# Optimization experiments

Hardware: AMD Instinct MI355X
Metric: run time of the kernel (lower is better)

## Reference

```python
import jax, jax.numpy as jnp
import numpy as np

N_HEADS = 16
NEG_INF = -1e9


def setup_inputs() -> dict:
    key = jax.random.key(0)
    k1, k2 = jax.random.split(key)
    B, T, C = 2, 2048, 1024
    x = jax.random.normal(k1, (B, T, C), dtype=jnp.float32)
    mask = jnp.ones((B, T, T), dtype=bool)  # padding mask, broadcastable to (B,T,T)
    W_qkv = jax.random.normal(k2, (3 * C, C), dtype=jnp.float32) * (C ** -0.5)
    b_qkv = jnp.zeros((3 * C,), dtype=jnp.float32)
    return {"x": x, "mask": mask, "W_qkv": W_qkv, "b_qkv": b_qkv}


def reference(x, mask, W_qkv, b_qkv):
    B, T, C = x.shape
    H = N_HEADS
    hd = C // H
    scale = jnp.asarray(C, jnp.float32) ** -0.5  # registered buffer 'scale'

    qkv = x @ W_qkv.T + b_qkv  # (B,T,3C)
    q, k, v = jnp.split(qkv, 3, axis=2)
    q = q.reshape(B, T, H, hd).transpose(0, 2, 1, 3)  # (B,H,T,hd)
    k = k.reshape(B, T, H, hd).transpose(0, 2, 1, 3)
    v = v.reshape(B, T, H, hd).transpose(0, 2, 1, 3)

    # NOTE: original code divides by scale = C**-0.5, i.e. multiplies by sqrt(C).
    att = jnp.einsum("bhqd,bhkd->bhqk", q, k) / scale  # (B,H,T,T)

    causal = jnp.tril(jnp.ones((T, T), dtype=bool))  # causal_mask buffer
    m = mask[:, None, :, :] & causal  # (B,1,T,T) & (T,T) -> (B,1,T,T)
    att = jnp.where(m, att, NEG_INF)
    att = jax.nn.softmax(att, axis=-1)

    y = jnp.einsum("bhqk,bhkd->bhqd", att, v)  # (B,H,T,hd)
    return y.transpose(0, 2, 1, 3).reshape(B, T, C)
```

## Files before the change

### kernel.cpp

```cpp
#include <hip/hip_runtime.h>


#define T_SEQ 2048
#define CDIM  1024
#define NH    16
#define HD    64

typedef short bf16x8 __attribute__((ext_vector_type(8)));
typedef float f32x4  __attribute__((ext_vector_type(4)));

#if defined(__has_builtin) && __has_builtin(__builtin_amdgcn_exp2f)
#define EXP2F __builtin_amdgcn_exp2f
#else
#define EXP2F exp2f
#endif

#define QSCALE 46.16624130844683f

__device__ __forceinline__ ushort f2bf(float x) {
    uint32_t u = __float_as_uint(x);
    return (ushort)((u + 0x7FFFu + ((u >> 16) & 1u)) >> 16);
}
__device__ __forceinline__ float bf2f(ushort h) {
    return __uint_as_float(((uint32_t)h) << 16);
}
__device__ __forceinline__ uint2 pack4(ushort a, ushort b, ushort c, ushort d) {
    return make_uint2((uint32_t)a | ((uint32_t)b << 16),
                      (uint32_t)c | ((uint32_t)d << 16));
}
__device__ __forceinline__ void gload_lds16(const void* g, void* l) {
    __builtin_amdgcn_global_load_lds(
        (const __attribute__((address_space(1))) void*)g,
        (__attribute__((address_space(3))) void*)l, 16, 0, 0);
}

__global__ __launch_bounds__(256) void split_bf16(
    const float* __restrict__ in, ushort* __restrict__ hi,
    ushort* __restrict__ lo, int n4)
{
    const int i = blockIdx.x * 256 + threadIdx.x;
    if (i >= n4) return;
    const float4 v = ((const float4*)in)[i];
    ushort h0 = f2bf(v.x), h1 = f2bf(v.y), h2 = f2bf(v.z), h3 = f2bf(v.w);
    ushort l0 = f2bf(v.x - bf2f(h0)), l1 = f2bf(v.y - bf2f(h1));
    ushort l2 = f2bf(v.z - bf2f(h2)), l3 = f2bf(v.w - bf2f(h3));
    ((uint2*)hi)[i] = pack4(h0, h1, h2, h3);
    ((uint2*)lo)[i] = pack4(l0, l1, l2, l3);
}

__global__ __launch_bounds__(256, 3) void qkv_mfma(
    const ushort* __restrict__ wh, const ushort* __restrict__ wl,
    const ushort* __restrict__ xh, const ushort* __restrict__ xl,
    const float* __restrict__ bias,
    ushort* __restrict__ q_hi, ushort* __restrict__ q_lo,
    ushort* __restrict__ k_hi, ushort* __restrict__ k_lo,
    ushort* __restrict__ v_t)
{
    __shared__ ushort stage[4][4096];

    const int tid = threadIdx.x;
    const int ln  = tid & 63;
    const int wv  = tid >> 6;
    const int wf  = wv >> 1;
    const int wt  = wv & 1;
    const int bx  = blockIdx.x % 24;
    const int by  = blockIdx.x / 24;
    const int f0  = bx * 128;
    const int tk0 = by * 128;

    const int r  = wv * 16 + (ln >> 2);
    const int sw = (ln & 3) ^ ((r >> 1) & 3);
    const ushort* p0 = wh + (size_t)(f0 + r) * CDIM + sw * 8;
    const ushort* p1 = wl + (size_t)(f0 + r) * CDIM + sw * 8;
    const ushort* p2 = xh + (size_t)(tk0 + r) * CDIM + sw * 8;
    const ushort* p3 = xl + (size_t)(tk0 + r) * CDIM + sw * 8;
    const int ldso = wv * 512;

    const int sp   = (ln >> 4) ^ (((ln & 15) >> 1) & 3);
    const int aoff = (wf * 64 + (ln & 15)) * 32 + sp * 8;
    const int boff = (wt * 64 + (ln & 15)) * 32 + sp * 8;

    const int which = f0 >> 10;
    const int hh    = ((f0 + wf * 64) & 1023) >> 6;
    const int bb    = tk0 >> 11;
    const size_t bhI = (size_t)(bb * NH + hh);
    const int t0 = (tk0 & 2047) + wt * 64;

    f32x4 acc[4][4];
#pragma unroll
    for (int mi = 0; mi < 4; ++mi)
#pragma unroll
        for (int ni = 0; ni < 4; ++ni) acc[mi][ni] = (f32x4){0.f, 0.f, 0.f, 0.f};

    if (which < 2) {
        for (int k0 = 0; k0 < CDIM; k0 += 32) {
            __syncthreads();
            gload_lds16(p0 + k0,           &stage[0][ldso]);
            gload_lds16(p0 + k0 + 64*CDIM, &stage[0][ldso + 2048]);
            gload_lds16(p1 + k0,           &stage[1][ldso]);
            gload_lds16(p1 + k0 + 64*CDIM, &stage[1][ldso + 2048]);
            gload_lds16(p2 + k0,           &stage[2][ldso]);
            gload_lds16(p2 + k0 + 64*CDIM, &stage[2][ldso + 2048]);
            gload_lds16(p3 + k0,           &stage[3][ldso]);
            gload_lds16(p3 + k0 + 64*CDIM, &stage[3][ldso + 2048]);
            __syncthreads();

            bf16x8 bh4[4], bl4[4];
#pragma unroll
            for (int ni = 0; ni < 4; ++ni) {
                bh4[ni] = *(const bf16x8*)&stage[2][boff + ni * 512];
                bl4[ni] = *(const bf16x8*)&stage[3][boff + ni * 512];
            }
#pragma unroll
            for (int mi = 0; mi < 4; ++mi) {
                const bf16x8 ah = *(const bf16x8*)&stage[0][aoff + mi * 512];
                const bf16x8 al = *(const bf16x8*)&stage[1][aoff + mi * 512];
#pragma unroll
                for (int ni = 0; ni < 4; ++ni) {
                    acc[mi][ni] = __builtin_amdgcn_mfma_f32_16x16x32_bf16(ah, bh4[ni], acc[mi][ni], 0, 0, 0);
                    acc[mi][ni] = __builtin_amdgcn_mfma_f32_16x16x32_bf16(ah, bl4[ni], acc[mi][ni], 0, 0, 0);
                    acc[mi][ni] = __builtin_amdgcn_mfma_f32_16x16x32_bf16(al, bh4[ni], acc[mi][ni], 0, 0, 0);
                }
            }
        }

        const float SC = (which == 0) ? QSCALE : 1.0f;
        ushort* oh = (which == 0) ? q_hi : k_hi;
        ushort* ol = (which == 0) ? q_lo : k_lo;
#pragma unroll
        for (int mi = 0; mi < 4; ++mi) {
            const int dql = mi * 16 + ((ln >> 4) << 2);
            const float4 b4 = *(const float4*)(bias + f0 + wf * 64 + dql);
            const float bbv[4] = {b4.x, b4.y, b4.z, b4.w};
#pragma unroll
            for (int ni = 0; ni < 4; ++ni) {
                const int t = t0 + ni * 16 + (ln & 15);
                ushort hs[4], ls[4];
#pragma unroll
                for (int jj = 0; jj < 4; ++jj) {
                    const float v = (acc[mi][ni][jj] + bbv[jj]) * SC;
                    hs[jj] = f2bf(v);
                    ls[jj] = f2bf(v - bf2f(hs[jj]));
                }
                const size_t idx = (bhI * T_SEQ + t) * HD + dql;
                *(uint2*)(oh + idx) = pack4(hs[0], hs[1], hs[2], hs[3]);
                *(uint2*)(ol + idx) = pack4(ls[0], ls[1], ls[2], ls[3]);
            }
        }
    } else {
        for (int k0 = 0; k0 < CDIM; k0 += 32) {
            __syncthreads();
            gload_lds16(p0 + k0,           &stage[0][ldso]);
            gload_lds16(p0 + k0 + 64*CDIM, &stage[0][ldso + 2048]);
            gload_lds16(p2 + k0,           &stage[2][ldso]);
            gload_lds16(p2 + k0 + 64*CDIM, &stage[2][ldso + 2048]);
            __syncthreads();

            bf16x8 bh4[4];
#pragma unroll
            for (int ni = 0; ni < 4; ++ni)
                bh4[ni] = *(const bf16x8*)&stage[2][boff + ni * 512];
#pragma unroll
            for (int mi = 0; mi < 4; ++mi) {
                const bf16x8 ah = *(const bf16x8*)&stage[0][aoff + mi * 512];
#pragma unroll
                for (int ni = 0; ni < 4; ++ni)
                    acc[mi][ni] = __builtin_amdgcn_mfma_f32_16x16x32_bf16(ah, bh4[ni], acc[mi][ni], 0, 0, 0);
            }
        }

#pragma unroll
        for (int mi = 0; mi < 4; ++mi) {
            const int dql = mi * 16 + ((ln >> 4) << 2);
            const float4 b4 = *(const float4*)(bias + f0 + wf * 64 + dql);
            const float bbv[4] = {b4.x, b4.y, b4.z, b4.w};
#pragma unroll
            for (int ni = 0; ni < 4; ++ni) {
                const int t = t0 + ni * 16 + (ln & 15);
#pragma unroll
                for (int jj = 0; jj < 4; ++jj) {
                    v_t[(bhI * HD + dql + jj) * T_SEQ + t] =
                        f2bf(acc[mi][ni][jj] + bbv[jj]);
                }
            }
        }
    }
}

__global__ __launch_bounds__(256, 2) void attn_mfma(
    const ushort* __restrict__ qh, const ushort* __restrict__ qlo,
    const ushort* __restrict__ kh, const ushort* __restrict__ klo,
    const ushort* __restrict__ vt, float* __restrict__ out)
{
    __shared__ ushort Kh_s[2][4096];
    __shared__ ushort Kl_s[2][4096];
    __shared__ ushort Vs[2][4096];
    __shared__ ushort Ps[4][1024];

    const int tid  = threadIdx.x;
    const int lane = tid & 63;
    const int wv   = tid >> 6;
    const int bh   = blockIdx.x & 31;
    const int j    = blockIdx.x >> 5;
    const int b    = bh >> 4, h = bh & 15;
    const int l15  = lane & 15;
    const int g    = lane >> 4;
    const int rsw  = l15 & 7;

    const size_t bhT = (size_t)bh * T_SEQ;
    const int qrow2[2] = { j * 64 + wv * 16 + l15,
                           (31 - j) * 64 + wv * 16 + l15 };
    const int nt = 32 - j;

    bf16x8 qb[2][2][2];
#pragma unroll
    for (int u = 0; u < 2; ++u) {
        const ushort* ph = qh  + ((bhT + qrow2[u]) << 6) + g * 8;
        const ushort* pl = qlo + ((bhT + qrow2[u]) << 6) + g * 8;
        qb[u][0][0] = *(const bf16x8*)(ph);
        qb[u][0][1] = *(const bf16x8*)(ph + 32);
        qb[u][1][0] = *(const bf16x8*)(pl);
        qb[u][1][1] = *(const bf16x8*)(pl + 32);
    }

    const int i8   = lane >> 3;
    const int sl   = lane & 7;
    const int ga   = sl ^ i8;
    const int row0 = wv * 16;

    f32x4 yacc[2][4];
#pragma unroll
    for (int u = 0; u < 2; ++u)
#pragma unroll
        for (int i = 0; i < 4; ++i) yacc[u][i] = (f32x4){0.f, 0.f, 0.f, 0.f};
    float mrun[2] = {-3.0e38f, -3.0e38f};
    float lrun[2] = {0.f, 0.f};

    ushort* Pl = Ps[wv];
    const int swz  = rsw << 3;
    const int prow = l15 * 64;

    auto stage = [&](int buf, int k0s) {
        const int ra = k0s + row0 + i8;
        const int rb = ra + 8;
        gload_lds16(kh  + ((bhT + ra) << 6) + ga * 8, &Kh_s[buf][row0 * 64]);
        gload_lds16(kh  + ((bhT + rb) << 6) + ga * 8, &Kh_s[buf][(row0 + 8) * 64]);
        gload_lds16(klo + ((bhT + ra) << 6) + ga * 8, &Kl_s[buf][row0 * 64]);
        gload_lds16(klo + ((bhT + rb) << 6) + ga * 8, &Kl_s[buf][(row0 + 8) * 64]);
        gload_lds16(vt + (size_t)(bh * HD + row0 + i8) * T_SEQ + k0s + ga * 8,
                    &Vs[buf][row0 * 64]);
        gload_lds16(vt + (size_t)(bh * HD + row0 + 8 + i8) * T_SEQ + k0s + ga * 8,
                    &Vs[buf][(row0 + 8) * 64]);
    };

    int cur = 0;
    stage(0, 0);

    for (int kt = 0; kt < nt; ++kt) {
        const int k0 = kt * 64;
        if (kt + 1 < nt) {
            stage(cur ^ 1, k0 + 64);
            asm volatile("s_waitcnt vmcnt(6)" ::: "memory");
        } else {
            asm volatile("s_waitcnt vmcnt(0)" ::: "memory");
        }
        __builtin_amdgcn_s_barrier();
        __builtin_amdgcn_sched_barrier(0);

        const bool aA = (kt <= j);

        f32x4 sacc[2][4];
#pragma unroll
        for (int u = 0; u < 2; ++u)
#pragma unroll
            for (int m = 0; m < 4; ++m) sacc[u][m] = (f32x4){0.f, 0.f, 0.f, 0.f};

#pragma unroll
        for (int m = 0; m < 4; ++m) {
            const int ro = (16 * m + l15) * 64;
            const bf16x8 ah0 = *(const bf16x8*)&Kh_s[cur][ro + ((g ^ rsw) << 3)];
            const bf16x8 ah1 = *(const bf16x8*)&Kh_s[cur][ro + (((4 + g) ^ rsw) << 3)];
            const bf16x8 al0 = *(const bf16x8*)&Kl_s[cur][ro + ((g ^ rsw) << 3)];
            const bf16x8 al1 = *(const bf16x8*)&Kl_s[cur][ro + (((4 + g) ^ rsw) << 3)];
#pragma unroll
            for (int u = 0; u < 2; ++u) {
                if (u == 0 && !aA) continue;
                sacc[u][m] = __builtin_amdgcn_mfma_f32_16x16x32_bf16(ah0, qb[u][0][0], sacc[u][m], 0, 0, 0);
                sacc[u][m] = __builtin_amdgcn_mfma_f32_16x16x32_bf16(ah1, qb[u][0][1], sacc[u][m], 0, 0, 0);
                sacc[u][m] = __builtin_amdgcn_mfma_f32_16x16x32_bf16(ah0, qb[u][1][0], sacc[u][m], 0, 0, 0);
                sacc[u][m] = __builtin_amdgcn_mfma_f32_16x16x32_bf16(ah1, qb[u][1][1], sacc[u][m], 0, 0, 0);
                sacc[u][m] = __builtin_amdgcn_mfma_f32_16x16x32_bf16(al0, qb[u][0][0], sacc[u][m], 0, 0, 0);
                sacc[u][m] = __builtin_amdgcn_mfma_f32_16x16x32_bf16(al1, qb[u][0][1], sacc[u][m], 0, 0, 0);
            }
        }

#pragma unroll
        for (int u = 0; u < 2; ++u) {
            if (u == 0 && !aA) continue;
            const int qrow = qrow2[u];
            const bool dm = (kt == (u ? nt - 1 : j));
            if (dm) {
#pragma unroll
                for (int m = 0; m < 4; ++m)
#pragma unroll
                    for (int rr = 0; rr < 4; ++rr)
                        if (k0 + 16 * m + 4 * g + rr > qrow) sacc[u][m][rr] = -3.0e38f;
            }

            float pmax = sacc[u][0][0];
#pragma unroll
            for (int m = 0; m < 4; ++m)
#pragma unroll
                for (int rr = 0; rr < 4; ++rr) pmax = fmaxf(pmax, sacc[u][m][rr]);
            pmax = fmaxf(pmax, __shfl_xor(pmax, 16));
            pmax = fmaxf(pmax, __shfl_xor(pmax, 32));
            const float mnew = fmaxf(mrun[u], pmax);
            const float sc = EXP2F(mrun[u] - mnew);

            float p[4][4];
            float ps = 0.f;
#pragma unroll
            for (int m = 0; m < 4; ++m)
#pragma unroll
                for (int rr = 0; rr < 4; ++rr) {
                    p[m][rr] = EXP2F(sacc[u][m][rr] - mnew);
                    ps += p[m][rr];
                }
            ps += __shfl_xor(ps, 16);
            ps += __shfl_xor(ps, 32);
            lrun[u] = lrun[u] * sc + ps;
            mrun[u] = mnew;

#pragma unroll
            for (int m = 0; m < 4; ++m) {
                const uint32_t w0 =
                    (uint32_t)f2bf(p[m][0]) | ((uint32_t)f2bf(p[m][1]) << 16);
                const uint32_t w1 =
                    (uint32_t)f2bf(p[m][2]) | ((uint32_t)f2bf(p[m][3]) << 16);
                const int kl0 = 16 * m + 4 * g;
                *(uint32_t*)&Pl[(prow + kl0)     ^ swz] = w0;
                *(uint32_t*)&Pl[(prow + kl0 + 2) ^ swz] = w1;
            }

#pragma unroll
            for (int f = 0; f < 4; ++f) yacc[u][f] *= sc;

#pragma unroll
            for (int s = 0; s < 2; ++s) {
                const bf16x8 pf = *(const bf16x8*)&Pl[(prow + 32 * s + 8 * g) ^ swz];
#pragma unroll
                for (int md = 0; md < 4; ++md) {
                    const bf16x8 vf = *(const bf16x8*)
                        &Vs[cur][(16 * md + l15) * 64 + (((4 * s + g) ^ rsw) << 3)];
                    yacc[u][md] = __builtin_amdgcn_mfma_f32_16x16x32_bf16(vf, pf, yacc[u][md], 0, 0, 0);
                }
            }
        }

        __builtin_amdgcn_s_barrier();
        cur ^= 1;
    }

#pragma unroll
    for (int u = 0; u < 2; ++u) {
        const float invl = 1.0f / lrun[u];
        float* op = out + (((size_t)b * T_SEQ + qrow2[u]) << 10) + h * HD + 4 * g;
#pragma unroll
        for (int md = 0; md < 4; ++md) {
            f32x4 o = yacc[u][md] * invl;
            *(f32x4*)(op + 16 * md) = o;
        }
    }
}

extern "C" void kernel_launch(void* const* d_in, const int* in_sizes, int n_in,
                              void* d_out, int out_size, void* d_ws, size_t ws_size,
                              hipStream_t stream)
{
    const float* x    = (const float*)d_in[0];
    const float* W    = (const float*)d_in[2];
    const float* bias = (const float*)d_in[3];
    float* out = (float*)d_out;

    const size_t per  = (size_t)2 * NH * T_SEQ * HD;
    const size_t wsz  = (size_t)3 * CDIM * CDIM;
    ushort* q_hi = (ushort*)d_ws;
    ushort* q_lo = q_hi + per;
    ushort* k_hi = q_lo + per;
    ushort* k_lo = k_hi + per;
    ushort* v_t  = k_lo + per;
    ushort* x_hi = v_t  + per;
    ushort* x_lo = x_hi + per;
    ushort* w_hi = x_lo + per;
    ushort* w_lo = w_hi + wsz;

    split_bf16<<<4096, 256, 0, stream>>>(x, x_hi, x_lo, 1048576);
    split_bf16<<<3072, 256, 0, stream>>>(W, w_hi, w_lo, 786432);
    qkv_mfma<<<24 * 32, 256, 0, stream>>>(w_hi, w_lo, x_hi, x_lo, bias,
                                          q_hi, q_lo, k_hi, k_lo, v_t);
    attn_mfma<<<16 * 32, 256, 0, stream>>>(q_hi, q_lo, k_hi, k_lo, v_t, out);
}
```

Baseline: 130.1 us.

## Double-buffer LDS staging in QKV projection GEMM with async prefetch

Converts the QKV projection kernel's K-loop into a two-stage software pipeline. The next K-slice is issued into a second LDS buffer before computing on the current one, with explicit vmcnt waits and raw s_barriers replacing the two __syncthreads per iteration. The aim is to hide global-to-LDS load latency behind the MFMA work. LDS use doubles to 64KB per block and the occupancy hint drops from 3 to 2 blocks, so fewer waves are resident.

```diff
diff --git a/kernel.cpp b/kernel.cpp
--- a/kernel.cpp
+++ b/kernel.cpp
@@ -48,7 +48,7 @@
     ((uint2*)lo)[i] = pack4(l0, l1, l2, l3);
 }
 
-__global__ __launch_bounds__(256, 3) void qkv_mfma(
+__global__ __launch_bounds__(256, 2) void qkv_mfma(
     const ushort* __restrict__ wh, const ushort* __restrict__ wl,
     const ushort* __restrict__ xh, const ushort* __restrict__ xl,
     const float* __restrict__ bias,
@@ -56,7 +56,7 @@
     ushort* __restrict__ k_hi, ushort* __restrict__ k_lo,
     ushort* __restrict__ v_t)
 {
-    __shared__ ushort stage[4][4096];
+    __shared__ ushort stage[2][4][4096];
 
     const int tid = threadIdx.x;
     const int ln  = tid & 63;
@@ -93,28 +93,39 @@
         for (int ni = 0; ni < 4; ++ni) acc[mi][ni] = (f32x4){0.f, 0.f, 0.f, 0.f};
 
     if (which < 2) {
-        for (int k0 = 0; k0 < CDIM; k0 += 32) {
-            __syncthreads();
-            gload_lds16(p0 + k0,           &stage[0][ldso]);
-            gload_lds16(p0 + k0 + 64*CDIM, &stage[0][ldso + 2048]);
-            gload_lds16(p1 + k0,           &stage[1][ldso]);
-            gload_lds16(p1 + k0 + 64*CDIM, &stage[1][ldso + 2048]);
-            gload_lds16(p2 + k0,           &stage[2][ldso]);
-            gload_lds16(p2 + k0 + 64*CDIM, &stage[2][ldso + 2048]);
-            gload_lds16(p3 + k0,           &stage[3][ldso]);
-            gload_lds16(p3 + k0 + 64*CDIM, &stage[3][ldso + 2048]);
-            __syncthreads();
+        auto stageQK = [&](int buf, int k0) {
+            gload_lds16(p0 + k0,           &stage[buf][0][ldso]);
+            gload_lds16(p0 + k0 + 64*CDIM, &stage[buf][0][ldso + 2048]);
+            gload_lds16(p1 + k0,           &stage[buf][1][ldso]);
+            gload_lds16(p1 + k0 + 64*CDIM, &stage[buf][1][ldso + 2048]);
+            gload_lds16(p2 + k0,           &stage[buf][2][ldso]);
+            gload_lds16(p2 + k0 + 64*CDIM, &stage[buf][2][ldso + 2048]);
+            gload_lds16(p3 + k0,           &stage[buf][3][ldso]);
+            gload_lds16(p3 + k0 + 64*CDIM, &stage[buf][3][ldso + 2048]);
+        };
+
+        stageQK(0, 0);
+        int buf = 0;
+        for (int k0 = 0; k0 < CDIM; k0 += 32, buf ^= 1) {
+            if (k0 + 32 < CDIM) {
+                stageQK(buf ^ 1, k0 + 32);
+                asm volatile("s_waitcnt vmcnt(8)" ::: "memory");
+            } else {
+                asm volatile("s_waitcnt vmcnt(0)" ::: "memory");
+            }
+            __builtin_amdgcn_s_barrier();
+            __builtin_amdgcn_sched_barrier(0);
 
             bf16x8 bh4[4], bl4[4];
 #pragma unroll
             for (int ni = 0; ni < 4; ++ni) {
-                bh4[ni] = *(const bf16x8*)&stage[2][boff + ni * 512];
-                bl4[ni] = *(const bf16x8*)&stage[3][boff + ni * 512];
+                bh4[ni] = *(const bf16x8*)&stage[buf][2][boff + ni * 512];
+                bl4[ni] = *(const bf16x8*)&stage[buf][3][boff + ni * 512];
             }
 #pragma unroll
             for (int mi = 0; mi < 4; ++mi) {
-                const bf16x8 ah = *(const bf16x8*)&stage[0][aoff + mi * 512];
-                const bf16x8 al = *(const bf16x8*)&stage[1][aoff + mi * 512];
+                const bf16x8 ah = *(const bf16x8*)&stage[buf][0][aoff + mi * 512];
+                const bf16x8 al = *(const bf16x8*)&stage[buf][1][aoff + mi * 512];
 #pragma unroll
                 for (int ni = 0; ni < 4; ++ni) {
                     acc[mi][ni] = __builtin_amdgcn_mfma_f32_16x16x32_bf16(ah, bh4[ni], acc[mi][ni], 0, 0, 0);
@@ -122,6 +133,7 @@
                     acc[mi][ni] = __builtin_amdgcn_mfma_f32_16x16x32_bf16(al, bh4[ni], acc[mi][ni], 0, 0, 0);
                 }
             }
+            __builtin_amdgcn_s_barrier();
         }
 
         const float SC = (which == 0) ? QSCALE : 1.0f;
@@ -148,25 +160,37 @@
             }
         }
     } else {
-        for (int k0 = 0; k0 < CDIM; k0 += 32) {
-            __syncthreads();
-            gload_lds16(p0 + k0,           &stage[0][ldso]);
-            gload_lds16(p0 + k0 + 64*CDIM, &stage[0][ldso + 2048]);
-            gload_lds16(p2 + k0,           &stage[2][ldso]);
-            gload_lds16(p2 + k0 + 64*CDIM, &stage[2][ldso + 2048]);
-            __syncthreads();
+        auto stageV = [&](int buf, int k0) {
+            gload_lds16(p0 + k0,           &stage[buf][0][ldso]);
+            gload_lds16(p0 + k0 + 64*CDIM, &stage[buf][0][ldso + 2048]);
+            gload_lds16(p2 + k0,           &stage[buf][2][ldso]);
+            gload_lds16(p2 + k0 + 64*CDIM, &stage[buf][2][ldso + 2048]);
+        };
+
+        stageV(0, 0);
+        int buf = 0;
+        for (int k0 = 0; k0 < CDIM; k0 += 32, buf ^= 1) {
+            if (k0 + 32 < CDIM) {
+                stageV(buf ^ 1, k0 + 32);
+                asm volatile("s_waitcnt vmcnt(4)" ::: "memory");
+            } else {
+                asm volatile("s_waitcnt vmcnt(0)" ::: "memory");
+            }
+            __builtin_amdgcn_s_barrier();
+            __builtin_amdgcn_sched_barrier(0);
 
             bf16x8 bh4[4];
 #pragma unroll
             for (int ni = 0; ni < 4; ++ni)
-                bh4[ni] = *(const bf16x8*)&stage[2][boff + ni * 512];
+                bh4[ni] = *(const bf16x8*)&stage[buf][2][boff + ni * 512];
 #pragma unroll
             for (int mi = 0; mi < 4; ++mi) {
-                const bf16x8 ah = *(const bf16x8*)&stage[0][aoff + mi * 512];
+                const bf16x8 ah = *(const bf16x8*)&stage[buf][0][aoff + mi * 512];
 #pragma unroll
                 for (int ni = 0; ni < 4; ++ni)
                     acc[mi][ni] = __builtin_amdgcn_mfma_f32_16x16x32_bf16(ah, bh4[ni], acc[mi][ni], 0, 0, 0);
             }
+            __builtin_amdgcn_s_barrier();
         }
 
 #pragma unroll
```

New measurement: 149.2 us. 14.7% more time.

## Split paired causal q-tiles into one tile per block, load V directly

Applied to the files above, without the earlier changes.

The attention kernel no longer pairs two query tiles per block to balance causal work. It now launches one block per 64-row query tile and orders the tiles in a heavy/light interleaved pattern. V fragments are read straight from global memory into registers instead of being staged through LDS, which frees shared memory, and launch bounds are raised to allow four blocks per CU. This trades per-block K reuse across two query tiles and LDS-coalesced V loads for more occupancy and less register pressure. The exposed global V load latency could hurt.

```diff
diff --git a/kernel.cpp b/kernel.cpp
--- a/kernel.cpp
+++ b/kernel.cpp
@@ -187,40 +187,39 @@
     }
 }
 
-__global__ __launch_bounds__(256, 2) void attn_mfma(
+__global__ __launch_bounds__(256, 4) void attn_mfma(
     const ushort* __restrict__ qh, const ushort* __restrict__ qlo,
     const ushort* __restrict__ kh, const ushort* __restrict__ klo,
     const ushort* __restrict__ vt, float* __restrict__ out)
 {
     __shared__ ushort Kh_s[2][4096];
     __shared__ ushort Kl_s[2][4096];
-    __shared__ ushort Vs[2][4096];
     __shared__ ushort Ps[4][1024];
 
     const int tid  = threadIdx.x;
     const int lane = tid & 63;
     const int wv   = tid >> 6;
     const int bh   = blockIdx.x & 31;
-    const int j    = blockIdx.x >> 5;
+    const int p    = blockIdx.x >> 5;
+    const int qt   = (p < 8) ? (31 - p) : (p < 16) ? (p - 8)
+                   : (p < 24) ? (39 - p) : (p - 16);
     const int b    = bh >> 4, h = bh & 15;
     const int l15  = lane & 15;
     const int g    = lane >> 4;
     const int rsw  = l15 & 7;
 
     const size_t bhT = (size_t)bh * T_SEQ;
-    const int qrow2[2] = { j * 64 + wv * 16 + l15,
-                           (31 - j) * 64 + wv * 16 + l15 };
-    const int nt = 32 - j;
-
-    bf16x8 qb[2][2][2];
-#pragma unroll
-    for (int u = 0; u < 2; ++u) {
-        const ushort* ph = qh  + ((bhT + qrow2[u]) << 6) + g * 8;
-        const ushort* pl = qlo + ((bhT + qrow2[u]) << 6) + g * 8;
-        qb[u][0][0] = *(const bf16x8*)(ph);
-        qb[u][0][1] = *(const bf16x8*)(ph + 32);
-        qb[u][1][0] = *(const bf16x8*)(pl);
-        qb[u][1][1] = *(const bf16x8*)(pl + 32);
+    const int qrow = qt * 64 + wv * 16 + l15;
+    const int nt   = qt + 1;
+
+    bf16x8 qb[2][2];
+    {
+        const ushort* ph = qh  + ((bhT + qrow) << 6) + g * 8;
+        const ushort* pl = qlo + ((bhT + qrow) << 6) + g * 8;
+        qb[0][0] = *(const bf16x8*)(ph);
+        qb[0][1] = *(const bf16x8*)(ph + 32);
+        qb[1][0] = *(const bf16x8*)(pl);
+        qb[1][1] = *(const bf16x8*)(pl + 32);
     }
 
     const int i8   = lane >> 3;
@@ -228,13 +227,12 @@
     const int ga   = sl ^ i8;
     const int row0 = wv * 16;
 
-    f32x4 yacc[2][4];
-#pragma unroll
-    for (int u = 0; u < 2; ++u)
-#pragma unroll
-        for (int i = 0; i < 4; ++i) yacc[u][i] = (f32x4){0.f, 0.f, 0.f, 0.f};
-    float mrun[2] = {-3.0e38f, -3.0e38f};
-    float lrun[2] = {0.f, 0.f};
+    const ushort* vp = vt + ((size_t)(bh * HD + l15)) * T_SEQ + g * 8;
+
+    f32x4 yacc[4];
+#pragma unroll
+    for (int i = 0; i < 4; ++i) yacc[i] = (f32x4){0.f, 0.f, 0.f, 0.f};
+    float mrun = -3.0e38f, lrun = 0.f;
 
     ushort* Pl = Ps[wv];
     const int swz  = rsw << 3;
@@ -247,10 +245,6 @@
         gload_lds16(kh  + ((bhT + rb) << 6) + ga * 8, &Kh_s[buf][(row0 + 8) * 64]);
         gload_lds16(klo + ((bhT + ra) << 6) + ga * 8, &Kl_s[buf][row0 * 64]);
         gload_lds16(klo + ((bhT + rb) << 6) + ga * 8, &Kl_s[buf][(row0 + 8) * 64]);
-        gload_lds16(vt + (size_t)(bh * HD + row0 + i8) * T_SEQ + k0s + ga * 8,
-                    &Vs[buf][row0 * 64]);
-        gload_lds16(vt + (size_t)(bh * HD + row0 + 8 + i8) * T_SEQ + k0s + ga * 8,
-                    &Vs[buf][(row0 + 8) * 64]);
     };
 
     int cur = 0;
@@ -258,23 +252,27 @@
 
     for (int kt = 0; kt < nt; ++kt) {
         const int k0 = kt * 64;
+
+        bf16x8 vfr[2][4];
+#pragma unroll
+        for (int s = 0; s < 2; ++s)
+#pragma unroll
+            for (int md = 0; md < 4; ++md)
+                vfr[s][md] = *(const bf16x8*)(
+                    vp + (size_t)md * (16 * T_SEQ) + k0 + 32 * s);
+
         if (kt + 1 < nt) {
             stage(cur ^ 1, k0 + 64);
-            asm volatile("s_waitcnt vmcnt(6)" ::: "memory");
+            asm volatile("s_waitcnt vmcnt(4)" ::: "memory");
         } else {
             asm volatile("s_waitcnt vmcnt(0)" ::: "memory");
         }
         __builtin_amdgcn_s_barrier();
         __builtin_amdgcn_sched_barrier(0);
 
-        const bool aA = (kt <= j);
-
-        f32x4 sacc[2][4];
-#pragma unroll
-        for (int u = 0; u < 2; ++u)
-#pragma unroll
-            for (int m = 0; m < 4; ++m) sacc[u][m] = (f32x4){0.f, 0.f, 0.f, 0.f};
-
+        f32x4 sacc[4];
+#pragma unroll
+        for (int m = 0; m < 4; ++m) sacc[m] = (f32x4){0.f, 0.f, 0.f, 0.f};
 #pragma unroll
         for (int m = 0; m < 4; ++m) {
             const int ro = (16 * m + l15) * 64;
@@ -282,94 +280,78 @@
             const bf16x8 ah1 = *(const bf16x8*)&Kh_s[cur][ro + (((4 + g) ^ rsw) << 3)];
             const bf16x8 al0 = *(const bf16x8*)&Kl_s[cur][ro + ((g ^ rsw) << 3)];
             const bf16x8 al1 = *(const bf16x8*)&Kl_s[cur][ro + (((4 + g) ^ rsw) << 3)];
-#pragma unroll
-            for (int u = 0; u < 2; ++u) {
-                if (u == 0 && !aA) continue;
-                sacc[u][m] = __builtin_amdgcn_mfma_f32_16x16x32_bf16(ah0, qb[u][0][0], sacc[u][m], 0, 0, 0);
-                sacc[u][m] = __builtin_amdgcn_mfma_f32_16x16x32_bf16(ah1, qb[u][0][1], sacc[u][m], 0, 0, 0);
-                sacc[u][m] = __builtin_amdgcn_mfma_f32_16x16x32_bf16(ah0, qb[u][1][0], sacc[u][m], 0, 0, 0);
-                sacc[u][m] = __builtin_amdgcn_mfma_f32_16x16x32_bf16(ah1, qb[u][1][1], sacc[u][m], 0, 0, 0);
-                sacc[u][m] = __builtin_amdgcn_mfma_f32_16x16x32_bf16(al0, qb[u][0][0], sacc[u][m], 0, 0, 0);
-                sacc[u][m] = __builtin_amdgcn_mfma_f32_16x16x32_bf16(al1, qb[u][0][1], sacc[u][m], 0, 0, 0);
-            }
-        }
-
-#pragma unroll
-        for (int u = 0; u < 2; ++u) {
-            if (u == 0 && !aA) continue;
-            const int qrow = qrow2[u];
-            const bool dm = (kt == (u ? nt - 1 : j));
-            if (dm) {
-#pragma unroll
-                for (int m = 0; m < 4; ++m)
-#pragma unroll
-                    for (int rr = 0; rr < 4; ++rr)
-                        if (k0 + 16 * m + 4 * g + rr > qrow) sacc[u][m][rr] = -3.0e38f;
-            }
-
-            float pmax = sacc[u][0][0];
+            sacc[m] = __builtin_amdgcn_mfma_f32_16x16x32_bf16(ah0, qb[0][0], sacc[m], 0, 0, 0);
+            sacc[m] = __builtin_amdgcn_mfma_f32_16x16x32_bf16(ah1, qb[0][1], sacc[m], 0, 0, 0);
+            sacc[m] = __builtin_amdgcn_mfma_f32_16x16x32_bf16(ah0, qb[1][0], sacc[m], 0, 0, 0);
+            sacc[m] = __builtin_amdgcn_mfma_f32_16x16x32_bf16(ah1, qb[1][1], sacc[m], 0, 0, 0);
+            sacc[m] = __builtin_amdgcn_mfma_f32_16x16x32_bf16(al0, qb[0][0], sacc[m], 0, 0, 0);
+            sacc[m] = __builtin_amdgcn_mfma_f32_16x16x32_bf16(al1, qb[0][1], sacc[m], 0, 0, 0);
+        }
+
+        if (kt == nt - 1) {
 #pragma unroll
             for (int m = 0; m < 4; ++m)
 #pragma unroll
-                for (int rr = 0; rr < 4; ++rr) pmax = fmaxf(pmax, sacc[u][m][rr]);
-            pmax = fmaxf(pmax, __shfl_xor(pmax, 16));
-            pmax = fmaxf(pmax, __shfl_xor(pmax, 32));
-            const float mnew = fmaxf(mrun[u], pmax);
-            const float sc = EXP2F(mrun[u] - mnew);
-
-            float p[4][4];
-            float ps = 0.f;
-#pragma unroll
-            for (int m = 0; m < 4; ++m)
-#pragma unroll
-                for (int rr = 0; rr < 4; ++rr) {
-                    p[m][rr] = EXP2F(sacc[u][m][rr] - mnew);
-                    ps += p[m][rr];
-                }
-            ps += __shfl_xor(ps, 16);
-            ps += __shfl_xor(ps, 32);
-            lrun[u] = lrun[u] * sc + ps;
-            mrun[u] = mnew;
-
-#pragma unroll
-            for (int m = 0; m < 4; ++m) {
-                const uint32_t w0 =
-                    (uint32_t)f2bf(p[m][0]) | ((uint32_t)f2bf(p[m][1]) << 16);
-                const uint32_t w1 =
-                    (uint32_t)f2bf(p[m][2]) | ((uint32_t)f2bf(p[m][3]) << 16);
-                const int kl0 = 16 * m + 4 * g;
-                *(uint32_t*)&Pl[(prow + kl0)     ^ swz] = w0;
-                *(uint32_t*)&Pl[(prow + kl0 + 2) ^ swz] = w1;
-            }
-
-#pragma unroll
-            for (int f = 0; f < 4; ++f) yacc[u][f] *= sc;
-
-#pragma unroll
-            for (int s = 0; s < 2; ++s) {
-                const bf16x8 pf = *(const bf16x8*)&Pl[(prow + 32 * s + 8 * g) ^ swz];
-#pragma unroll
-                for (int md = 0; md < 4; ++md) {
-                    const bf16x8 vf = *(const bf16x8*)
-                        &Vs[cur][(16 * md + l15) * 64 + (((4 * s + g) ^ rsw) << 3)];
-                    yacc[u][md] = __builtin_amdgcn_mfma_f32_16x16x32_bf16(vf, pf, yacc[u][md], 0, 0, 0);
-                }
-            }
+                for (int rr = 0; rr < 4; ++rr)
+                    if (k0 + 16 * m + 4 * g + rr > qrow) sacc[m][rr] = -3.0e38f;
+        }
+
+        float pmax = sacc[0][0];
+#pragma unroll
+        for (int m = 0; m < 4; ++m)
+#pragma unroll
+            for (int rr = 0; rr < 4; ++rr) pmax = fmaxf(pmax, sacc[m][rr]);
+        pmax = fmaxf(pmax, __shfl_xor(pmax, 16));
+        pmax = fmaxf(pmax, __shfl_xor(pmax, 32));
+        const float mnew = fmaxf(mrun, pmax);
+        const float sc = EXP2F(mrun - mnew);
+
+        float pv[4][4];
+        float ps = 0.f;
+#pragma unroll
+        for (int m = 0; m < 4; ++m)
+#pragma unroll
+            for (int rr = 0; rr < 4; ++rr) {
+                pv[m][rr] = EXP2F(sacc[m][rr] - mnew);
+                ps += pv[m][rr];
+            }
+        ps += __shfl_xor(ps, 16);
+        ps += __shfl_xor(ps, 32);
+        lrun = lrun * sc + ps;
+        mrun = mnew;
+
+#pragma unroll
+        for (int m = 0; m < 4; ++m) {
+            const uint32_t w0 =
+                (uint32_t)f2bf(pv[m][0]) | ((uint32_t)f2bf(pv[m][1]) << 16);
+            const uint32_t w1 =
+                (uint32_t)f2bf(pv[m][2]) | ((uint32_t)f2bf(pv[m][3]) << 16);
+            const int kl0 = 16 * m + 4 * g;
+            *(uint32_t*)&Pl[(prow + kl0)     ^ swz] = w0;
+            *(uint32_t*)&Pl[(prow + kl0 + 2) ^ swz] = w1;
+        }
+
+#pragma unroll
+        for (int f = 0; f < 4; ++f) yacc[f] *= sc;
+
+#pragma unroll
+        for (int s = 0; s < 2; ++s) {
+            const bf16x8 pf = *(const bf16x8*)&Pl[(prow + 32 * s + 8 * g) ^ swz];
+#pragma unroll
+            for (int md = 0; md < 4; ++md)
+                yacc[md] = __builtin_amdgcn_mfma_f32_16x16x32_bf16(vfr[s][md], pf, yacc[md], 0, 0, 0);
         }
 
         __builtin_amdgcn_s_barrier();
         cur ^= 1;
     }
 
-#pragma unroll
-    for (int u = 0; u < 2; ++u) {
-        const float invl = 1.0f / lrun[u];
-        float* op = out + (((size_t)b * T_SEQ + qrow2[u]) << 10) + h * HD + 4 * g;
-#pragma unroll
-        for (int md = 0; md < 4; ++md) {
-            f32x4 o = yacc[u][md] * invl;
-            *(f32x4*)(op + 16 * md) = o;
-        }
+    const float invl = 1.0f / lrun;
+    float* op = out + (((size_t)b * T_SEQ + qrow) << 10) + h * HD + 4 * g;
+#pragma unroll
+    for (int md = 0; md < 4; ++md) {
+        f32x4 o = yacc[md] * invl;
+        *(f32x4*)(op + 16 * md) = o;
     }
 }
 
@@ -398,5 +380,5 @@
     split_bf16<<<3072, 256, 0, stream>>>(W, w_hi, w_lo, 786432);
     qkv_mfma<<<24 * 32, 256, 0, stream>>>(w_hi, w_lo, x_hi, x_lo, bias,
                                           q_hi, q_lo, k_hi, k_lo, v_t);
-    attn_mfma<<<16 * 32, 256, 0, stream>>>(q_hi, q_lo, k_hi, k_lo, v_t, out);
-}
+    attn_mfma<<<32 * 32, 256, 0, stream>>>(q_hi, q_lo, k_hi, k_lo, v_t, out);
+}
```

Result: slower. 158.6 us (+21.9%).
